# Kernel optimization log

Hardware: AMD Instinct MI355X
Metric: run time of the kernel (lower is better)

The kernel has to match this reference:

```python
import jax, jax.numpy as jnp
import numpy as np

NUM_ELECTRODES = 19
NUM_WINDOWS = 30
NUM_FREQS = 128
HEADS = 8
HID = 80
BATCH = 16
D_OUT = HEADS * HID  # 640


def _build_edge_index(num_nodes, num_windows):
    # spatiotemporal graph: dense intra-window blocks (incl. self-loops)
    # + bidirectional temporal edges between same electrode in adjacent windows
    srcs, dsts = [], []
    for w in range(num_windows):
        idx = np.arange(num_nodes) + w * num_nodes
        s, d = np.meshgrid(idx, idx, indexing='ij')
        srcs.append(s.ravel()); dsts.append(d.ravel())
    for w in range(num_windows - 1):
        a = np.arange(num_nodes) + w * num_nodes
        b = a + num_nodes
        srcs.append(a); dsts.append(b)
        srcs.append(b); dsts.append(a)
    return np.stack([np.concatenate(srcs), np.concatenate(dsts)]).astype(np.int32)


def setup_inputs() -> dict:
    key = jax.random.key(0)
    ks = jax.random.split(key, 12)
    f = NUM_FREQS
    x = jax.random.normal(ks[0], (BATCH, NUM_WINDOWS, NUM_FREQS, NUM_ELECTRODES), jnp.float32)
    s_in = 1.0 / np.sqrt(f)
    s_h = 1.0 / np.sqrt(D_OUT)
    Wl = jax.random.normal(ks[1], (D_OUT, f), jnp.float32) * s_in
    bl = jax.random.normal(ks[2], (D_OUT,), jnp.float32) * s_in
    Wr = jax.random.normal(ks[3], (D_OUT, f), jnp.float32) * s_in
    br = jax.random.normal(ks[4], (D_OUT,), jnp.float32) * s_in
    att = jax.random.normal(ks[5], (HEADS, HID), jnp.float32) * (1.0 / np.sqrt(HID))
    conv_bias = jax.random.normal(ks[6], (D_OUT,), jnp.float32) * 0.01
    Wpool = jax.random.normal(ks[7], (1, D_OUT), jnp.float32) * s_h
    bpool = jax.random.normal(ks[8], (1,), jnp.float32) * s_h
    Wfc = jax.random.normal(ks[9], (1, D_OUT), jnp.float32) * s_h
    bfc = jax.random.normal(ks[10], (1,), jnp.float32) * s_h
    edge_index = jnp.asarray(_build_edge_index(NUM_ELECTRODES, NUM_WINDOWS))
    return {"x": x, "edge_index": edge_index, "Wl": Wl, "bl": bl, "Wr": Wr, "br": br,
            "att": att, "conv_bias": conv_bias, "Wpool": Wpool, "bpool": bpool,
            "Wfc": Wfc, "bfc": bfc}


def reference(x, edge_index, Wl, bl, Wr, br, att, conv_bias, Wpool, bpool, Wfc, bfc):
    B, W, F, E19 = x.shape
    N = W * E19
    H, C = att.shape
    # (B, W, F, E) -> (B, W, E, F) -> (B, N, F)
    nodes = x.transpose(0, 1, 3, 2).reshape(B, N, F)
    src, dst = edge_index[0], edge_index[1]
    # GATv2: lin_l on source (messages), lin_r on target
    xl = (nodes @ Wl.T + bl).reshape(B, N, H, C)
    xr = (nodes @ Wr.T + br).reshape(B, N, H, C)
    msg = xl[:, src]                        # (B, E, H, C) source features
    key_feat = msg + xr[:, dst]             # (B, E, H, C)
    e = jnp.einsum('behc,hc->beh', jax.nn.leaky_relu(key_feat, 0.2), att)  # (B,E,H)

    def seg_softmax(e_b):  # (E, H), segment softmax over dst
        m = jax.ops.segment_max(e_b, dst, num_segments=N)
        ex = jnp.exp(e_b - m[dst])
        s = jax.ops.segment_sum(ex, dst, num_segments=N)
        return ex / (s[dst] + 1e-16)

    alpha = jax.vmap(seg_softmax)(e)        # (B, E, H)
    agg = jax.vmap(lambda m: jax.ops.segment_sum(m, dst, num_segments=N))(
        msg * alpha[..., None])             # (B, N, H, C)
    out = agg.reshape(B, N, H * C) + conv_bias
    out = jax.nn.elu(out)
    scores = out @ Wpool.T + bpool          # (B, N, 1)
    attn = jax.nn.softmax(scores, axis=1)
    pooled = (attn * out).sum(axis=1)       # (B, H*C)
    logits = pooled @ Wfc.T + bfc           # (B, 1)
    return logits.squeeze(1)
```

## Files before the change

kernel.cpp:

```cpp
#include <hip/hip_runtime.h>
#include <math.h>

#define B   16
#define NW  30
#define NE  19
#define NF  128
#define NH  8
#define NC  80
#define ND  640
#define NN  570
#define NROW (B*NN)

typedef _Float16 f16x2 __attribute__((ext_vector_type(2)));
typedef _Float16 f16x4 __attribute__((ext_vector_type(4)));
typedef _Float16 f16x8 __attribute__((ext_vector_type(8)));
typedef float    f32x16 __attribute__((ext_vector_type(16)));

#define WT_OFF   0
#define WT_SZ    (1280*128)
#define XL_OFF   (WT_OFF + WT_SZ)
#define XLR16_SZ (B*NN*ND/2)
#define XR_OFF   (XL_OFF + XLR16_SZ)
#define XT_OFF   (XR_OFF + XLR16_SZ)
#define SCP_OFF  (XT_OFF + 2*(NROW*NF/2))
#define SCP_SZ   (NH*B*NN)
#define QP_OFF   (SCP_OFF + SCP_SZ)

__device__ __forceinline__ void load_lds16(const void* g, void* l){
#if __has_builtin(__builtin_amdgcn_global_load_lds)
  __builtin_amdgcn_global_load_lds(
      (const __attribute__((address_space(1))) unsigned int*)g,
      (__attribute__((address_space(3))) unsigned int*)l, 16, 0, 0);
#else
  *(f16x8*)l = *(const f16x8*)g;
#endif
}

__device__ __forceinline__ float dot8(f16x8 zm, f16x8 a8, float acc){
#if __has_builtin(__builtin_amdgcn_fdot2)
  acc = __builtin_amdgcn_fdot2(__builtin_shufflevector(zm, zm, 0, 1),
                               __builtin_shufflevector(a8, a8, 0, 1), acc, false);
  acc = __builtin_amdgcn_fdot2(__builtin_shufflevector(zm, zm, 2, 3),
                               __builtin_shufflevector(a8, a8, 2, 3), acc, false);
  acc = __builtin_amdgcn_fdot2(__builtin_shufflevector(zm, zm, 4, 5),
                               __builtin_shufflevector(a8, a8, 4, 5), acc, false);
  acc = __builtin_amdgcn_fdot2(__builtin_shufflevector(zm, zm, 6, 7),
                               __builtin_shufflevector(a8, a8, 6, 7), acc, false);
#else
  #pragma unroll
  for (int j = 0; j < 8; ++j) acc = fmaf((float)zm[j], (float)a8[j], acc);
#endif
  return acc;
}

__global__ __launch_bounds__(256) void k0_prep(const float* __restrict__ Wl,
                                               const float* __restrict__ Wr,
                                               const float* __restrict__ x,
                                               _Float16* __restrict__ wph,
                                               _Float16* __restrict__ wpl,
                                               _Float16* __restrict__ xph,
                                               _Float16* __restrict__ xpl){
  int bx = blockIdx.x, t = threadIdx.x;
  if (bx < 160){
    int i = bx*256 + t;
    int dd = i >> 5, k = (i & 31) * 4;
    const float* srcp = (dd < 640) ? (Wl + dd*NF + k) : (Wr + (dd-640)*NF + k);
    float4 v = *(const float4*)srcp;
    _Float16 h0=(_Float16)v.x, h1=(_Float16)v.y, h2=(_Float16)v.z, h3=(_Float16)v.w;
    f16x4 hv = {h0, h1, h2, h3};
    f16x4 lv = {(_Float16)(v.x-(float)h0), (_Float16)(v.y-(float)h1),
                (_Float16)(v.z-(float)h2), (_Float16)(v.w-(float)h3)};
    int s = k >> 4, hh = (k >> 3) & 1, off = k & 7;
    size_t chunk = (((size_t)(dd >> 5)*8 + s)*64 + hh*32 + (dd & 31))*8 + off;
    *(f16x4*)(wph + chunk) = hv;
    *(f16x4*)(wpl + chunk) = lv;
    return;
  }
  int wb = bx - 160, w = wb % NW, b = wb / NW;
  __shared__ float ns[19*132];
  const float4* xs = (const float4*)(x + (size_t)((b*NW + w)*NF)*NE);
  for (int i = t; i < 608; i += 256){
    float4 v = xs[i];
    int idx = 4*i;
    float vv[4] = {v.x, v.y, v.z, v.w};
    #pragma unroll
    for (int k = 0; k < 4; ++k){
      int f = (idx + k) / NE, el = (idx + k) % NE;
      ns[el*132 + f] = vv[k];
    }
  }
  __syncthreads();
  for (int i = t; i < 608; i += 256){
    int el = i >> 5, k = (i & 31) * 4;
    float4 v = *(const float4*)&ns[el*132 + k];
    _Float16 h0=(_Float16)v.x, h1=(_Float16)v.y, h2=(_Float16)v.z, h3=(_Float16)v.w;
    f16x4 hv = {h0, h1, h2, h3};
    f16x4 lv = {(_Float16)(v.x-(float)h0), (_Float16)(v.y-(float)h1),
                (_Float16)(v.z-(float)h2), (_Float16)(v.w-(float)h3)};
    int n = (b*NW + w)*NE + el;
    int s = k >> 4, hh = (k >> 3) & 1, off = k & 7;
    size_t chunk = (((size_t)(n >> 5)*8 + s)*64 + hh*32 + (n & 31))*8 + off;
    *(f16x4*)(xph + chunk) = hv;
    *(f16x4*)(xpl + chunk) = lv;
  }
}

__global__ __launch_bounds__(256) void k1_gemm(const _Float16* __restrict__ xph,
                                               const _Float16* __restrict__ xpl,
                                               const _Float16* __restrict__ wph,
                                               const _Float16* __restrict__ wpl,
                                               const float* __restrict__ bl,
                                               const float* __restrict__ br,
                                               _Float16* __restrict__ xl,
                                               _Float16* __restrict__ xr){
  int t = threadIdx.x;
  int wave = t >> 6, lane = t & 63;
  int mt = blockIdx.x;
  int nt = blockIdx.y*4 + wave;

  __shared__ _Float16 ash[4096];
  __shared__ _Float16 asl[4096];
  {
    const f16x8* gh = (const f16x8*)(xph + (size_t)mt*4096);
    const f16x8* gl = (const f16x8*)(xpl + (size_t)mt*4096);
    #pragma unroll
    for (int c = 0; c < 2; ++c){
      ((f16x8*)ash)[t + c*256] = gh[t + c*256];
      ((f16x8*)asl)[t + c*256] = gl[t + c*256];
    }
  }
  __syncthreads();

  const f16x8* sah = (const f16x8*)ash + lane;
  const f16x8* sal = (const f16x8*)asl + lane;
  const f16x8* pbh = (const f16x8*)wph + (size_t)nt*8*64 + lane;
  const f16x8* pbl = (const f16x8*)wpl + (size_t)nt*8*64 + lane;

  f32x16 acc = {};
  #pragma unroll
  for (int s = 0; s < 8; ++s){
    f16x8 a_h = sah[s*64];
    f16x8 b_h = pbh[s*64];
    f16x8 a_l = sal[s*64];
    f16x8 b_l = pbl[s*64];
    acc = __builtin_amdgcn_mfma_f32_32x32x16_f16(a_h, b_h, acc, 0, 0, 0);
    acc = __builtin_amdgcn_mfma_f32_32x32x16_f16(a_l, b_h, acc, 0, 0, 0);
    acc = __builtin_amdgcn_mfma_f32_32x32x16_f16(a_h, b_l, acc, 0, 0, 0);
  }

  int bn = nt*32 + (lane & 31);
  bool isl = bn < 640;
  int col = isl ? bn : bn - 640;
  float bias = isl ? bl[bn] : br[col];
  _Float16* dstb = isl ? xl : xr;
  int h = col / 80, c = col % 80;
  int rbase = mt*32 + 4*(lane >> 5);
  #pragma unroll
  for (int r = 0; r < 16; ++r){
    int row = rbase + (r & 3) + 8*(r >> 2);
    int bb = row / 570, n = row - bb*570;
    dstb[((size_t)(h*B + bb)*NN + n)*80 + c] = (_Float16)(acc[r] + bias);
  }
}

__global__ __launch_bounds__(256) void k2_gat(const _Float16* __restrict__ xl,
                                              const _Float16* __restrict__ xr,
                                              const float* __restrict__ att,
                                              const float* __restrict__ cb,
                                              const float* __restrict__ wpool,
                                              const float* __restrict__ wfc,
                                              float* __restrict__ scp,
                                              float* __restrict__ qp){
  int t = threadIdx.x;
  int wg = blockIdx.x + NW*(blockIdx.y + B*blockIdx.z);
  int idx = (wg & 7)*480 + (wg >> 3);
  int w = idx % NW, rem = idx / NW;
  int b = rem % B, h = rem / B;

  __shared__ __attribute__((aligned(16))) _Float16 xl_s[57*80];
  __shared__ _Float16 xr_s[19*88];
  __shared__ _Float16 atth_s[80];
  __shared__ float cb_s[80], wp_s[80], wf_s[80];
  __shared__ float e_s[19*22];
  __shared__ float score_s[19], q_s[19];
  if (t < 19){ score_s[t] = 0.f; q_s[t] = 0.f; }
  const bool vp = (w > 0), vn = (w < NW-1);
  const int own0 = vp ? 19 : 0;
  const int nrows = 19 + (vp ? 19 : 0) + (vn ? 19 : 0);
  const int lo = (vp ? w-1 : w)*NE;

  const _Float16* xsrc = xl + ((size_t)(h*B + b)*NN + lo)*80;
  for (int i = t; i < nrows*10; i += 256)
    load_lds16(xsrc + i*8, &xl_s[i*8]);
  const _Float16* rsrc = xr + ((size_t)(h*B + b)*NN + (size_t)w*NE)*80;
  for (int i = t; i < 190; i += 256){
    int row = i / 10, c8 = i % 10;
    *(f16x8*)&xr_s[row*88 + 8*c8] = *(const f16x8*)(rsrc + row*80 + 8*c8);
  }
  if (t < 80){
    int a = t / 20, c4 = t % 20;
    if (a == 0){
      float4 v = *(const float4*)(att + h*80 + 4*c4);
      f16x4 hv = {(_Float16)v.x, (_Float16)v.y, (_Float16)v.z, (_Float16)v.w};
      *(f16x4*)&atth_s[4*c4] = hv;
    } else {
      const float* sp0 = (a == 1) ? cb + h*80 : (a == 2) ? wpool + h*80 : wfc + h*80;
      float*       dp  = (a == 1) ? cb_s      : (a == 2) ? wp_s        : wf_s;
      *(float4*)&dp[4*c4] = *(const float4*)(sp0 + 4*c4);
    }
  }
  __syncthreads();

  for (int eid = t; eid < 399; eid += 256){
    int s = eid / 19, dst = eid % 19;
    if ((s == 19 && !vp) || (s == 20 && !vn)) continue;
    int row = (s < 19) ? own0 + s : (s == 19 ? dst : own0 + 19 + dst);
    const f16x8* xlp = (const f16x8*)&xl_s[row*80];
    const f16x8* xrp = (const f16x8*)&xr_s[dst*88];
    const f16x8* ap  = (const f16x8*)atth_s;
    float acc = 0.f;
    #pragma unroll 2
    for (int c8 = 0; c8 < 10; ++c8){
      f16x8 z  = xlp[c8] + xrp[c8];
      f16x8 zm = __builtin_elementwise_max(z, z * (_Float16)0.2f);
      acc = dot8(zm, ap[c8], acc);
    }
    e_s[dst*22 + s] = acc;
  }
  __syncthreads();

  if (t < 19){
    float* base = &e_s[t*22];
    float m = -1e30f;
    for (int s = 0; s < 21; ++s){
      if ((s == 19 && !vp) || (s == 20 && !vn)) continue;
      m = fmaxf(m, base[s]);
    }
    float sum = 0.f;
    for (int s = 0; s < 21; ++s){
      if ((s == 19 && !vp) || (s == 20 && !vn)) continue;
      float ex = __expf(base[s] - m); base[s] = ex; sum += ex;
    }
    base[21] = 1.f / (sum + 1e-16f);
  }
  __syncthreads();

  if (t < 190){
    int dst = t / 10, c0 = (t % 10) * 8;
    float acc[8];
    #pragma unroll
    for (int j = 0; j < 8; ++j) acc[j] = 0.f;
    for (int s = 0; s < 21; ++s){
      if ((s == 19 && !vp) || (s == 20 && !vn)) continue;
      int row = (s < 19) ? own0 + s : (s == 19 ? dst : own0 + 19 + dst);
      float al = e_s[dst*22 + s];
      f16x8 v = *(const f16x8*)&xl_s[row*80 + c0];
      #pragma unroll
      for (int j = 0; j < 8; ++j) acc[j] = fmaf(al, (float)v[j], acc[j]);
    }
    float inv = e_s[dst*22 + 21];
    float sp = 0.f, fq = 0.f;
    #pragma unroll
    for (int k = 0; k < 8; ++k){
      float v = fmaf(inv, acc[k], cb_s[c0 + k]);
      v = (v > 0.f) ? v : (__expf(v) - 1.f);
      sp += v * wp_s[c0 + k];
      fq += v * wf_s[c0 + k];
    }
    atomicAdd(&score_s[dst], sp);
    atomicAdd(&q_s[dst], fq);
  }
  __syncthreads();
  if (t < 19){
    size_t o = ((size_t)h*B + b)*NN + (size_t)w*NE + t;
    scp[o] = score_s[t];
    qp[o]  = q_s[t];
  }
}

__global__ __launch_bounds__(256) void k3_final(const float* __restrict__ scp,
                                                const float* __restrict__ qp,
                                                const float* __restrict__ bpool,
                                                const float* __restrict__ bfc,
                                                float* __restrict__ out){
  int b = blockIdx.x, t = threadIdx.x;
  __shared__ float ss[NN], qq[NN];
  __shared__ float red[4], rs[4], rq[4];
  float bp = bpool[0];
  for (int i = t; i < NN; i += 256){
    float v = bp, q = 0.f;
    #pragma unroll
    for (int h = 0; h < NH; ++h){
      v += scp[((size_t)h*B + b)*NN + i];
      q += qp [((size_t)h*B + b)*NN + i];
    }
    ss[i] = v; qq[i] = q;
  }
  __syncthreads();
  float m = -1e30f;
  for (int i = t; i < NN; i += 256) m = fmaxf(m, ss[i]);
  for (int off = 32; off > 0; off >>= 1) m = fmaxf(m, __shfl_down(m, off));
  int wid = t >> 6, lane = t & 63;
  if (lane == 0) red[wid] = m;
  __syncthreads();
  if (t == 0) red[0] = fmaxf(fmaxf(red[0], red[1]), fmaxf(red[2], red[3]));
  __syncthreads();
  m = red[0];
  float s = 0.f, qs = 0.f;
  for (int i = t; i < NN; i += 256){
    float e = __expf(ss[i] - m);
    s += e; qs += e * qq[i];
  }
  for (int off = 32; off > 0; off >>= 1){
    s  += __shfl_down(s, off);
    qs += __shfl_down(qs, off);
  }
  if (lane == 0){ rs[wid] = s; rq[wid] = qs; }
  __syncthreads();
  if (t == 0){
    float S = rs[0] + rs[1] + rs[2] + rs[3];
    float Q = rq[0] + rq[1] + rq[2] + rq[3];
    out[b] = Q / (S + 1e-16f) + bfc[0];
  }
}

extern "C" void kernel_launch(void* const* d_in, const int* in_sizes, int n_in,
                              void* d_out, int out_size, void* d_ws, size_t ws_size,
                              hipStream_t stream){
  const float* x     = (const float*)d_in[0];
  const float* Wl    = (const float*)d_in[2];
  const float* bl    = (const float*)d_in[3];
  const float* Wr    = (const float*)d_in[4];
  const float* br    = (const float*)d_in[5];
  const float* att   = (const float*)d_in[6];
  const float* cb    = (const float*)d_in[7];
  const float* wpool = (const float*)d_in[8];
  const float* bpool = (const float*)d_in[9];
  const float* wfc   = (const float*)d_in[10];
  const float* bfc   = (const float*)d_in[11];

  float* ws      = (float*)d_ws;
  _Float16* wph  = (_Float16*)(ws + WT_OFF);
  _Float16* wpl  = wph + 1280*NF;
  _Float16* xlb  = (_Float16*)(ws + XL_OFF);
  _Float16* xrb  = (_Float16*)(ws + XR_OFF);
  _Float16* xph  = (_Float16*)(ws + XT_OFF);
  _Float16* xpl  = xph + (size_t)NROW*NF;
  float* scp     = ws + SCP_OFF;
  float* qp      = ws + QP_OFF;

  k0_prep  <<<640, 256, 0, stream>>>(Wl, Wr, x, wph, wpl, xph, xpl);
  k1_gemm  <<<dim3(285, 10), 256, 0, stream>>>(xph, xpl, wph, wpl, bl, br, xlb, xrb);
  k2_gat   <<<dim3(NW, B, NH), 256, 0, stream>>>(xlb, xrb, att, cb, wpool, wfc, scp, qp);
  k3_final <<<B, 256, 0, stream>>>(scp, qp, bpool, bfc, (float*)d_out);
}
```

Baseline: 142.5 us.

## Map each GAT window to one wavefront and read xl directly from global

The GAT kernel now gives each (head, batch, window) unit to a single 64-lane wavefront, with four units per block, instead of a full 256-thread block. Block-wide barriers become wave-local LDS fences. The shared-memory staging of the 57 xl rows is dropped: source features are read straight from global memory (relying on cache), and xr rows are held in registers. This is meant to cut idle threads and barrier overhead, at the cost of repeated global reads and higher register pressure.

```diff
diff --git a/kernel.cpp b/kernel.cpp
--- a/kernel.cpp
+++ b/kernel.cpp
@@ -25,16 +25,6 @@
 #define SCP_OFF  (XT_OFF + 2*(NROW*NF/2))
 #define SCP_SZ   (NH*B*NN)
 #define QP_OFF   (SCP_OFF + SCP_SZ)
-
-__device__ __forceinline__ void load_lds16(const void* g, void* l){
-#if __has_builtin(__builtin_amdgcn_global_load_lds)
-  __builtin_amdgcn_global_load_lds(
-      (const __attribute__((address_space(1))) unsigned int*)g,
-      (__attribute__((address_space(3))) unsigned int*)l, 16, 0, 0);
-#else
-  *(f16x8*)l = *(const f16x8*)g;
-#endif
-}
 
 __device__ __forceinline__ float dot8(f16x8 zm, f16x8 a8, float acc){
 #if __has_builtin(__builtin_amdgcn_fdot2)
@@ -51,6 +41,11 @@
   for (int j = 0; j < 8; ++j) acc = fmaf((float)zm[j], (float)a8[j], acc);
 #endif
   return acc;
+}
+
+__device__ __forceinline__ void wave_lds_fence(){
+  asm volatile("s_waitcnt lgkmcnt(0)" ::: "memory");
+  __builtin_amdgcn_wave_barrier();
 }
 
 __global__ __launch_bounds__(256) void k0_prep(const float* __restrict__ Wl,
@@ -171,66 +166,68 @@
                                               const float* __restrict__ wfc,
                                               float* __restrict__ scp,
                                               float* __restrict__ qp){
-  int t = threadIdx.x;
-  int wg = blockIdx.x + NW*(blockIdx.y + B*blockIdx.z);
-  int idx = (wg & 7)*480 + (wg >> 3);
-  int w = idx % NW, rem = idx / NW;
-  int b = rem % B, h = rem / B;
-
-  __shared__ __attribute__((aligned(16))) _Float16 xl_s[57*80];
-  __shared__ _Float16 xr_s[19*88];
-  __shared__ _Float16 atth_s[80];
-  __shared__ float cb_s[80], wp_s[80], wf_s[80];
-  __shared__ float e_s[19*22];
-  __shared__ float score_s[19], q_s[19];
-  if (t < 19){ score_s[t] = 0.f; q_s[t] = 0.f; }
+  int t = threadIdx.x, wv = t >> 6, lane = t & 63;
+  int bx = blockIdx.x;
+  int h = bx & 7;
+  int u = (bx >> 3)*4 + wv;
+  int w = u % NW, b = u / NW;
+
+  __shared__ _Float16 atth[4][80];
+  __shared__ float cbs[4][80], wps[4][80], wfs[4][80];
+  __shared__ float es[4][19*22];
+  __shared__ float scs[4][20], qqs[4][20];
+
   const bool vp = (w > 0), vn = (w < NW-1);
   const int own0 = vp ? 19 : 0;
-  const int nrows = 19 + (vp ? 19 : 0) + (vn ? 19 : 0);
   const int lo = (vp ? w-1 : w)*NE;
-
-  const _Float16* xsrc = xl + ((size_t)(h*B + b)*NN + lo)*80;
-  for (int i = t; i < nrows*10; i += 256)
-    load_lds16(xsrc + i*8, &xl_s[i*8]);
-  const _Float16* rsrc = xr + ((size_t)(h*B + b)*NN + (size_t)w*NE)*80;
-  for (int i = t; i < 190; i += 256){
-    int row = i / 10, c8 = i % 10;
-    *(f16x8*)&xr_s[row*88 + 8*c8] = *(const f16x8*)(rsrc + row*80 + 8*c8);
-  }
-  if (t < 80){
-    int a = t / 20, c4 = t % 20;
+  const _Float16* xbase = xl + ((size_t)(h*B + b)*NN + lo)*80;
+  const _Float16* rsrc  = xr + ((size_t)(h*B + b)*NN + (size_t)w*NE)*80;
+
+  if (lane < 19){ scs[wv][lane] = 0.f; qqs[wv][lane] = 0.f; }
+  for (int i = lane; i < 80; i += 64){
+    int a = i / 20, c4 = i % 20;
     if (a == 0){
       float4 v = *(const float4*)(att + h*80 + 4*c4);
       f16x4 hv = {(_Float16)v.x, (_Float16)v.y, (_Float16)v.z, (_Float16)v.w};
-      *(f16x4*)&atth_s[4*c4] = hv;
+      *(f16x4*)&atth[wv][4*c4] = hv;
     } else {
-      const float* sp0 = (a == 1) ? cb + h*80 : (a == 2) ? wpool + h*80 : wfc + h*80;
-      float*       dp  = (a == 1) ? cb_s      : (a == 2) ? wp_s        : wf_s;
-      *(float4*)&dp[4*c4] = *(const float4*)(sp0 + 4*c4);
-    }
-  }
-  __syncthreads();
-
-  for (int eid = t; eid < 399; eid += 256){
-    int s = eid / 19, dst = eid % 19;
-    if ((s == 19 && !vp) || (s == 20 && !vn)) continue;
-    int row = (s < 19) ? own0 + s : (s == 19 ? dst : own0 + 19 + dst);
-    const f16x8* xlp = (const f16x8*)&xl_s[row*80];
-    const f16x8* xrp = (const f16x8*)&xr_s[dst*88];
-    const f16x8* ap  = (const f16x8*)atth_s;
-    float acc = 0.f;
-    #pragma unroll 2
-    for (int c8 = 0; c8 < 10; ++c8){
-      f16x8 z  = xlp[c8] + xrp[c8];
-      f16x8 zm = __builtin_elementwise_max(z, z * (_Float16)0.2f);
-      acc = dot8(zm, ap[c8], acc);
-    }
-    e_s[dst*22 + s] = acc;
-  }
-  __syncthreads();
-
-  if (t < 19){
-    float* base = &e_s[t*22];
+      const float* s0 = (a == 1) ? cb + h*80 : (a == 2) ? wpool + h*80 : wfc + h*80;
+      float*       dp = (a == 1) ? cbs[wv]   : (a == 2) ? wps[wv]      : wfs[wv];
+      *(float4*)&dp[4*c4] = *(const float4*)(s0 + 4*c4);
+    }
+  }
+
+  int dst = lane % 19;
+  int sg  = lane / 19;
+  f16x8 xrr[10];
+  #pragma unroll
+  for (int c8 = 0; c8 < 10; ++c8)
+    xrr[c8] = *(const f16x8*)(rsrc + dst*80 + 8*c8);
+
+  wave_lds_fence();
+
+  if (sg < 3){
+    #pragma unroll
+    for (int k = 0; k < 7; ++k){
+      int s = sg*7 + k;
+      if ((s == 19 && !vp) || (s == 20 && !vn)) continue;
+      int row = (s < 19) ? own0 + s : (s == 19 ? dst : own0 + 19 + dst);
+      const f16x8* xp = (const f16x8*)(xbase + row*80);
+      const f16x8* ap = (const f16x8*)atth[wv];
+      float acc = 0.f;
+      #pragma unroll 2
+      for (int c8 = 0; c8 < 10; ++c8){
+        f16x8 z  = xp[c8] + xrr[c8];
+        f16x8 zm = __builtin_elementwise_max(z, z * (_Float16)0.2f);
+        acc = dot8(zm, ap[c8], acc);
+      }
+      es[wv][dst*22 + s] = acc;
+    }
+  }
+  wave_lds_fence();
+
+  if (lane < 19){
+    float* base = &es[wv][lane*22];
     float m = -1e30f;
     for (int s = 0; s < 21; ++s){
       if ((s == 19 && !vp) || (s == 20 && !vn)) continue;
@@ -243,38 +240,43 @@
     }
     base[21] = 1.f / (sum + 1e-16f);
   }
-  __syncthreads();
-
-  if (t < 190){
-    int dst = t / 10, c0 = (t % 10) * 8;
-    float acc[8];
-    #pragma unroll
-    for (int j = 0; j < 8; ++j) acc[j] = 0.f;
-    for (int s = 0; s < 21; ++s){
-      if ((s == 19 && !vp) || (s == 20 && !vn)) continue;
-      int row = (s < 19) ? own0 + s : (s == 19 ? dst : own0 + 19 + dst);
-      float al = e_s[dst*22 + s];
-      f16x8 v = *(const f16x8*)&xl_s[row*80 + c0];
+  wave_lds_fence();
+
+  for (int r = 0; r < 3; ++r){
+    int item = r*64 + lane;
+    if (item < 190){
+      int d2 = item / 10, c8 = item % 10;
+      float acc[8];
       #pragma unroll
-      for (int j = 0; j < 8; ++j) acc[j] = fmaf(al, (float)v[j], acc[j]);
-    }
-    float inv = e_s[dst*22 + 21];
-    float sp = 0.f, fq = 0.f;
-    #pragma unroll
-    for (int k = 0; k < 8; ++k){
-      float v = fmaf(inv, acc[k], cb_s[c0 + k]);
-      v = (v > 0.f) ? v : (__expf(v) - 1.f);
-      sp += v * wp_s[c0 + k];
-      fq += v * wf_s[c0 + k];
-    }
-    atomicAdd(&score_s[dst], sp);
-    atomicAdd(&q_s[dst], fq);
-  }
-  __syncthreads();
-  if (t < 19){
-    size_t o = ((size_t)h*B + b)*NN + (size_t)w*NE + t;
-    scp[o] = score_s[t];
-    qp[o]  = q_s[t];
+      for (int j = 0; j < 8; ++j) acc[j] = 0.f;
+      for (int s = 0; s < 21; ++s){
+        if ((s == 19 && !vp) || (s == 20 && !vn)) continue;
+        int row = (s < 19) ? own0 + s : (s == 19 ? d2 : own0 + 19 + d2);
+        float al = es[wv][d2*22 + s];
+        f16x8 v = *(const f16x8*)(xbase + row*80 + c8*8);
+        #pragma unroll
+        for (int j = 0; j < 8; ++j) acc[j] = fmaf(al, (float)v[j], acc[j]);
+      }
+      float inv = es[wv][d2*22 + 21];
+      float sp = 0.f, fq = 0.f;
+      #pragma unroll
+      for (int k = 0; k < 8; ++k){
+        int c0 = c8*8 + k;
+        float v = fmaf(inv, acc[k], cbs[wv][c0]);
+        v = (v > 0.f) ? v : (__expf(v) - 1.f);
+        sp += v * wps[wv][c0];
+        fq += v * wfs[wv][c0];
+      }
+      atomicAdd(&scs[wv][d2], sp);
+      atomicAdd(&qqs[wv][d2], fq);
+    }
+  }
+  wave_lds_fence();
+
+  if (lane < 19){
+    size_t o = ((size_t)h*B + b)*NN + (size_t)w*NE + lane;
+    scp[o] = scs[wv][lane];
+    qp[o]  = qqs[wv][lane];
   }
 }
 
@@ -351,6 +353,6 @@
 
   k0_prep  <<<640, 256, 0, stream>>>(Wl, Wr, x, wph, wpl, xph, xpl);
   k1_gemm  <<<dim3(285, 10), 256, 0, stream>>>(xph, xpl, wph, wpl, bl, br, xlb, xrb);
-  k2_gat   <<<dim3(NW, B, NH), 256, 0, stream>>>(xlb, xrb, att, cb, wpool, wfc, scp, qp);
+  k2_gat   <<<960, 256, 0, stream>>>(xlb, xrb, att, cb, wpool, wfc, scp, qp);
   k3_final <<<B, 256, 0, stream>>>(scp, qp, bpool, bfc, (float*)d_out);
 }
```

Result: slower. 172.4 us (+21.0%).

## Process three windows per GAT workgroup to reuse halo xl rows

Applied to the files above, without the earlier changes.

The GAT kernel now assigns three consecutive windows to each workgroup, loading up to 95 xl rows and 57 xr rows once instead of reloading the neighbouring-window halo rows for every window. The grid shrinks from 30 to 10 blocks along the window axis, and each block runs the three windows one after another with barriers in between. This cuts redundant global loads and per-block setup, but it drops the custom XCD-aware block remapping, lowers parallelism to 1280 blocks, and serialises the per-window phases within each block.

```diff
diff --git a/kernel.cpp b/kernel.cpp
--- a/kernel.cpp
+++ b/kernel.cpp
@@ -171,110 +171,116 @@
                                               const float* __restrict__ wfc,
                                               float* __restrict__ scp,
                                               float* __restrict__ qp){
-  int t = threadIdx.x;
-  int wg = blockIdx.x + NW*(blockIdx.y + B*blockIdx.z);
-  int idx = (wg & 7)*480 + (wg >> 3);
-  int w = idx % NW, rem = idx / NW;
-  int b = rem % B, h = rem / B;
-
-  __shared__ __attribute__((aligned(16))) _Float16 xl_s[57*80];
-  __shared__ _Float16 xr_s[19*88];
-  __shared__ _Float16 atth_s[80];
-  __shared__ float cb_s[80], wp_s[80], wf_s[80];
-  __shared__ float e_s[19*22];
-  __shared__ float score_s[19], q_s[19];
-  if (t < 19){ score_s[t] = 0.f; q_s[t] = 0.f; }
-  const bool vp = (w > 0), vn = (w < NW-1);
-  const int own0 = vp ? 19 : 0;
-  const int nrows = 19 + (vp ? 19 : 0) + (vn ? 19 : 0);
-  const int lo = (vp ? w-1 : w)*NE;
-
-  const _Float16* xsrc = xl + ((size_t)(h*B + b)*NN + lo)*80;
-  for (int i = t; i < nrows*10; i += 256)
-    load_lds16(xsrc + i*8, &xl_s[i*8]);
-  const _Float16* rsrc = xr + ((size_t)(h*B + b)*NN + (size_t)w*NE)*80;
-  for (int i = t; i < 190; i += 256){
-    int row = i / 10, c8 = i % 10;
-    *(f16x8*)&xr_s[row*88 + 8*c8] = *(const f16x8*)(rsrc + row*80 + 8*c8);
+  int tr = blockIdx.x, b = blockIdx.y, h = blockIdx.z, t = threadIdx.x;
+  int w0 = tr*3;
+  int wlo = (tr == 0) ? 0 : (w0 - 1);
+  int nxl = ((tr == 0 || tr == 9) ? 76 : 95)*10;
+
+  __shared__ __attribute__((aligned(16))) _Float16 xls[95*80];
+  __shared__ _Float16 xrs[57*88];
+  __shared__ _Float16 atth[80];
+  __shared__ float cbs[80], wps[80], wfs[80];
+  __shared__ float es[19*22];
+  __shared__ float scs[3][19], qqs[3][19];
+
+  const _Float16* xsrc = xl + ((size_t)(h*B + b)*NN + (size_t)wlo*NE)*80;
+  const _Float16* rsrc = xr + ((size_t)(h*B + b)*NN + (size_t)w0*NE)*80;
+
+  for (int i = t; i < nxl; i += 256)
+    load_lds16(xsrc + i*8, &xls[i*8]);
+  for (int i = t; i < 570; i += 256){
+    int r = i/10, c = i%10;
+    *(f16x8*)&xrs[r*88 + c*8] = *(const f16x8*)(rsrc + i*8);
   }
   if (t < 80){
     int a = t / 20, c4 = t % 20;
     if (a == 0){
       float4 v = *(const float4*)(att + h*80 + 4*c4);
       f16x4 hv = {(_Float16)v.x, (_Float16)v.y, (_Float16)v.z, (_Float16)v.w};
-      *(f16x4*)&atth_s[4*c4] = hv;
+      *(f16x4*)&atth[4*c4] = hv;
     } else {
-      const float* sp0 = (a == 1) ? cb + h*80 : (a == 2) ? wpool + h*80 : wfc + h*80;
-      float*       dp  = (a == 1) ? cb_s      : (a == 2) ? wp_s        : wf_s;
-      *(float4*)&dp[4*c4] = *(const float4*)(sp0 + 4*c4);
-    }
-  }
-  __syncthreads();
-
-  for (int eid = t; eid < 399; eid += 256){
-    int s = eid / 19, dst = eid % 19;
-    if ((s == 19 && !vp) || (s == 20 && !vn)) continue;
-    int row = (s < 19) ? own0 + s : (s == 19 ? dst : own0 + 19 + dst);
-    const f16x8* xlp = (const f16x8*)&xl_s[row*80];
-    const f16x8* xrp = (const f16x8*)&xr_s[dst*88];
-    const f16x8* ap  = (const f16x8*)atth_s;
-    float acc = 0.f;
-    #pragma unroll 2
-    for (int c8 = 0; c8 < 10; ++c8){
-      f16x8 z  = xlp[c8] + xrp[c8];
-      f16x8 zm = __builtin_elementwise_max(z, z * (_Float16)0.2f);
-      acc = dot8(zm, ap[c8], acc);
-    }
-    e_s[dst*22 + s] = acc;
-  }
-  __syncthreads();
-
-  if (t < 19){
-    float* base = &e_s[t*22];
-    float m = -1e30f;
-    for (int s = 0; s < 21; ++s){
+      const float* s0 = (a == 1) ? cb + h*80 : (a == 2) ? wpool + h*80 : wfc + h*80;
+      float*       dp = (a == 1) ? cbs       : (a == 2) ? wps          : wfs;
+      *(float4*)&dp[4*c4] = *(const float4*)(s0 + 4*c4);
+    }
+  } else if (t < 137){
+    int u = t - 80;
+    scs[u/19][u%19] = 0.f; qqs[u/19][u%19] = 0.f;
+  }
+  __syncthreads();
+
+  #pragma unroll 1
+  for (int j = 0; j < 3; ++j){
+    int w = w0 + j;
+    const bool vp = (w > 0), vn = (w < NW-1);
+    const int ob = (w - wlo)*NE;
+
+    for (int eid = t; eid < 399; eid += 256){
+      int s = eid / 19, dst = eid % 19;
       if ((s == 19 && !vp) || (s == 20 && !vn)) continue;
-      m = fmaxf(m, base[s]);
-    }
-    float sum = 0.f;
-    for (int s = 0; s < 21; ++s){
-      if ((s == 19 && !vp) || (s == 20 && !vn)) continue;
-      float ex = __expf(base[s] - m); base[s] = ex; sum += ex;
-    }
-    base[21] = 1.f / (sum + 1e-16f);
-  }
-  __syncthreads();
-
-  if (t < 190){
-    int dst = t / 10, c0 = (t % 10) * 8;
-    float acc[8];
-    #pragma unroll
-    for (int j = 0; j < 8; ++j) acc[j] = 0.f;
-    for (int s = 0; s < 21; ++s){
-      if ((s == 19 && !vp) || (s == 20 && !vn)) continue;
-      int row = (s < 19) ? own0 + s : (s == 19 ? dst : own0 + 19 + dst);
-      float al = e_s[dst*22 + s];
-      f16x8 v = *(const f16x8*)&xl_s[row*80 + c0];
+      int row = (s < 19) ? ob + s : (s == 19 ? ob - NE + dst : ob + NE + dst);
+      const f16x8* xlp = (const f16x8*)&xls[row*80];
+      const f16x8* xrp = (const f16x8*)&xrs[(j*NE + dst)*88];
+      const f16x8* ap  = (const f16x8*)atth;
+      float acc = 0.f;
+      #pragma unroll 2
+      for (int c8 = 0; c8 < 10; ++c8){
+        f16x8 z  = xlp[c8] + xrp[c8];
+        f16x8 zm = __builtin_elementwise_max(z, z * (_Float16)0.2f);
+        acc = dot8(zm, ap[c8], acc);
+      }
+      es[dst*22 + s] = acc;
+    }
+    __syncthreads();
+
+    if (t < 19){
+      float* base = &es[t*22];
+      float m = -1e30f;
+      for (int s = 0; s < 21; ++s){
+        if ((s == 19 && !vp) || (s == 20 && !vn)) continue;
+        m = fmaxf(m, base[s]);
+      }
+      float sum = 0.f;
+      for (int s = 0; s < 21; ++s){
+        if ((s == 19 && !vp) || (s == 20 && !vn)) continue;
+        float ex = __expf(base[s] - m); base[s] = ex; sum += ex;
+      }
+      base[21] = 1.f / (sum + 1e-16f);
+    }
+    __syncthreads();
+
+    if (t < 190){
+      int dst = t / 10, c0 = (t % 10) * 8;
+      float acc[8];
       #pragma unroll
-      for (int j = 0; j < 8; ++j) acc[j] = fmaf(al, (float)v[j], acc[j]);
-    }
-    float inv = e_s[dst*22 + 21];
-    float sp = 0.f, fq = 0.f;
-    #pragma unroll
-    for (int k = 0; k < 8; ++k){
-      float v = fmaf(inv, acc[k], cb_s[c0 + k]);
-      v = (v > 0.f) ? v : (__expf(v) - 1.f);
-      sp += v * wp_s[c0 + k];
-      fq += v * wf_s[c0 + k];
-    }
-    atomicAdd(&score_s[dst], sp);
-    atomicAdd(&q_s[dst], fq);
-  }
-  __syncthreads();
-  if (t < 19){
-    size_t o = ((size_t)h*B + b)*NN + (size_t)w*NE + t;
-    scp[o] = score_s[t];
-    qp[o]  = q_s[t];
+      for (int jj = 0; jj < 8; ++jj) acc[jj] = 0.f;
+      for (int s = 0; s < 21; ++s){
+        if ((s == 19 && !vp) || (s == 20 && !vn)) continue;
+        int row = (s < 19) ? ob + s : (s == 19 ? ob - NE + dst : ob + NE + dst);
+        float al = es[dst*22 + s];
+        f16x8 v = *(const f16x8*)&xls[row*80 + c0];
+        #pragma unroll
+        for (int jj = 0; jj < 8; ++jj) acc[jj] = fmaf(al, (float)v[jj], acc[jj]);
+      }
+      float inv = es[dst*22 + 21];
+      float sp = 0.f, fq = 0.f;
+      #pragma unroll
+      for (int k = 0; k < 8; ++k){
+        float v = fmaf(inv, acc[k], cbs[c0 + k]);
+        v = (v > 0.f) ? v : (__expf(v) - 1.f);
+        sp += v * wps[c0 + k];
+        fq += v * wfs[c0 + k];
+      }
+      atomicAdd(&scs[j][dst], sp);
+      atomicAdd(&qqs[j][dst], fq);
+    }
+    __syncthreads();
+
+    if (t < 19){
+      size_t o = ((size_t)h*B + b)*NN + (size_t)w*NE + t;
+      scp[o] = scs[j][t];
+      qp[o]  = qqs[j][t];
+    }
   }
 }
 
@@ -351,6 +357,6 @@
 
   k0_prep  <<<640, 256, 0, stream>>>(Wl, Wr, x, wph, wpl, xph, xpl);
   k1_gemm  <<<dim3(285, 10), 256, 0, stream>>>(xph, xpl, wph, wpl, bl, br, xlb, xrb);
-  k2_gat   <<<dim3(NW, B, NH), 256, 0, stream>>>(xlb, xrb, att, cb, wpool, wfc, scp, qp);
+  k2_gat   <<<dim3(10, B, NH), 256, 0, stream>>>(xlb, xrb, att, cb, wpool, wfc, scp, qp);
   k3_final <<<B, 256, 0, stream>>>(scp, qp, bpool, bfc, (float*)d_out);
 }
```

Result: no change. 144.6 us (+1.5%).
